# Optimization experiments

Measured on AMD Instinct MI355X. Metric: run time of the kernel, lower is better.

Reference implementation:

```python
import jax, jax.numpy as jnp
import numpy as np

EMBED_DIM = 1024
NUM_HEADS = 16
HEAD_DIM = EMBED_DIM // NUM_HEADS


def setup_inputs() -> dict:
    key = jax.random.key(0)
    ks = jax.random.split(key, 12)
    B, S, D = 2, 2048, EMBED_DIM
    sc = 1.0 / np.sqrt(D)
    inp = {
        "query": jax.random.normal(ks[0], (B, S, D), jnp.float32),
        "key": jax.random.normal(ks[1], (B, S, D), jnp.float32),
        "value": jax.random.normal(ks[2], (B, S, D), jnp.float32),
        # causal mask: True = masked out (matches masked_fill semantics)
        "attn_mask": jnp.triu(jnp.ones((S, S), dtype=bool), k=1),
        "q_w": jax.random.normal(ks[3], (D, D), jnp.float32) * sc,
        "q_b": jnp.zeros((D,), jnp.float32),
        "k_w": jax.random.normal(ks[4], (D, D), jnp.float32) * sc,
        "k_b": jnp.zeros((D,), jnp.float32),
        "v_w": jax.random.normal(ks[5], (D, D), jnp.float32) * sc,
        "v_b": jnp.zeros((D,), jnp.float32),
        "o_w": jax.random.normal(ks[6], (D, D), jnp.float32) * sc,
        "o_b": jnp.zeros((D,), jnp.float32),
    }
    return inp


def reference(query, key, value, attn_mask, q_w, q_b, k_w, k_b, v_w, v_b, o_w, o_b):
    B, S, D = query.shape
    H, hd = NUM_HEADS, HEAD_DIM

    def proj(x, w, b):
        # nn.Linear: x @ w.T + b ; reshape to [B, H, S, hd]
        y = jnp.einsum('bsd,ed->bse', x, w) + b
        return y.reshape(B, S, H, hd).transpose(0, 2, 1, 3)

    Q = proj(query, q_w, q_b)
    K = proj(key, k_w, k_b)
    V = proj(value, v_w, v_b)

    scores = jnp.einsum('bhqd,bhkd->bhqk', Q, K) / jnp.sqrt(jnp.float32(hd))
    scores = jnp.where(attn_mask, jnp.float32(-1e9), scores)
    attn = jax.nn.softmax(scores, axis=-1)  # dropout=0.0 (eval)
    ctx = jnp.einsum('bhqk,bhkd->bhqd', attn, V)
    ctx = ctx.transpose(0, 2, 1, 3).reshape(B, S, D)
    out = jnp.einsum('bsd,ed->bse', ctx, o_w) + o_b
    return out
```

## Files before the change

### kernel.cpp

```cpp
#include <hip/hip_runtime.h>
#include <hip/hip_bf16.h>

typedef __bf16 bf16;
typedef __attribute__((ext_vector_type(8))) __bf16 bf16x8;
typedef __attribute__((ext_vector_type(4))) __bf16 bf16x4;
typedef __attribute__((ext_vector_type(4))) float f32x4;

struct CvtArgs {
  const float* src[7];
  bf16* dst[7];
  int n4[7];
};

__global__ __launch_bounds__(256) void cvt_kernel(CvtArgs a) {
  const int seg = blockIdx.y;
  const float4* s = (const float4*)a.src[seg];
  bf16x4* d = (bf16x4*)a.dst[seg];
  const int n = a.n4[seg];
  const int stride = gridDim.x * 256;
  for (int i = blockIdx.x * 256 + threadIdx.x; i < n; i += stride) {
    const float4 v = s[i];
    bf16x4 h;
    h[0] = (bf16)v.x; h[1] = (bf16)v.y; h[2] = (bf16)v.z; h[3] = (bf16)v.w;
    d[i] = h;
  }
}

__device__ __forceinline__ void gload16(const void* g, void* l) {
  __builtin_amdgcn_global_load_lds(
      (const __attribute__((address_space(1))) void*)g,
      (__attribute__((address_space(3))) void*)l, 16, 0, 0);
}

__device__ __forceinline__ void gemm_core2(const bf16* __restrict__ A,
                                           const bf16* __restrict__ W,
                                           const float* __restrict__ bias,
                                           void* __restrict__ C,
                                           float scale, int mode,
                                           int bx, int by) {
  constexpr int K = 1024, N = 1024, BK = 32, NT = K / BK;
  __shared__ __align__(16) bf16 As[3][128 * BK];
  __shared__ __align__(16) bf16 Bs[3][128 * BK];

  const int tid = threadIdx.x;
  const int lane = tid & 63;
  const int w = tid >> 6;
  const int wm = w >> 1, wn = w & 1;
  const int g = lane >> 4, c16 = lane & 15;
  const int row0 = by * 128;
  const int col0 = bx * 128;

  const int sr = tid >> 2;
  const int ssw = ((tid & 3) ^ (sr & 3)) * 8;
  const int sdst = tid * 8;

  const int aoff = (wm * 64 + c16) * BK + ((g ^ (c16 & 3)) * 8);
  const int boff = (wn * 64 + c16) * BK + ((g ^ (c16 & 3)) * 8);

  f32x4 acc[4][4] = {};

#define STAGE2(buf, kt)                                                          \
  {                                                                              \
    const int k0_ = (kt)*BK;                                                     \
    gload16(&A[(size_t)(row0 + sr) * K + k0_ + ssw], &As[buf][sdst]);            \
    gload16(&A[(size_t)(row0 + 64 + sr) * K + k0_ + ssw], &As[buf][2048 + sdst]);\
    gload16(&W[(size_t)(col0 + sr) * K + k0_ + ssw], &Bs[buf][sdst]);            \
    gload16(&W[(size_t)(col0 + 64 + sr) * K + k0_ + ssw], &Bs[buf][2048 + sdst]);\
  }

  STAGE2(0, 0);
  STAGE2(1, 1);

  int cur = 0;
#pragma unroll 1
  for (int kt = 0; kt < NT; ++kt) {
    if (kt == NT - 1)
      asm volatile("s_waitcnt vmcnt(0)" ::: "memory");
    else
      asm volatile("s_waitcnt vmcnt(4)" ::: "memory");
    __builtin_amdgcn_s_barrier();
    __builtin_amdgcn_sched_barrier(0);

    if (kt + 2 < NT) {
      const int nb = (cur + 2 >= 3) ? cur - 1 : cur + 2;
      STAGE2(nb, kt + 2);
    }

    bf16x8 a[4], b[4];
#pragma unroll
    for (int m = 0; m < 4; ++m) a[m] = *(const bf16x8*)&As[cur][aoff + m * 512];
#pragma unroll
    for (int n = 0; n < 4; ++n) b[n] = *(const bf16x8*)&Bs[cur][boff + n * 512];

    __builtin_amdgcn_s_setprio(1);
#pragma unroll
    for (int m = 0; m < 4; ++m)
#pragma unroll
      for (int n = 0; n < 4; ++n)
        acc[m][n] = __builtin_amdgcn_mfma_f32_16x16x32_bf16(a[m], b[n], acc[m][n], 0, 0, 0);
    __builtin_amdgcn_s_setprio(0);

    cur = (cur + 1 == 3) ? 0 : cur + 1;
  }
#undef STAGE2

#pragma unroll
  for (int m = 0; m < 4; ++m) {
#pragma unroll
    for (int n = 0; n < 4; ++n) {
      const int col = col0 + wn * 64 + n * 16 + c16;
      if (mode == 2) {
        const int row = row0 + wm * 64 + m * 16 + g * 4;
        const int bb = row >> 11, s = row & 2047;
        const int hh = col >> 6, j = col & 63;
        bf16x4 hv;
#pragma unroll
        for (int r = 0; r < 4; ++r)
          hv[r] = (bf16)((acc[m][n][r] + bias[col]) * scale);
        *(bf16x4*)&((bf16*)C)[(((size_t)bb * 16 + hh) * 64 + j) * 2048 + s] = hv;
      } else {
#pragma unroll
        for (int r = 0; r < 4; ++r) {
          const int row = row0 + wm * 64 + m * 16 + g * 4 + r;
          const float v = (acc[m][n][r] + bias[col]) * scale;
          if (mode == 1) {
            const int bb = row >> 11, s = row & 2047;
            const int hh = col >> 6, j = col & 63;
            ((bf16*)C)[(((size_t)bb * 16 + hh) * 2048 + s) * 64 + j] = (bf16)v;
          } else {
            ((float*)C)[(size_t)row * N + col] = v;
          }
        }
      }
    }
  }
}

__device__ __forceinline__ void xcd_swz(int& bx, int& by, int& bz) {
  const int lid = ((int)blockIdx.z * 32 + (int)blockIdx.y) * 8 + (int)blockIdx.x;
  const int cpx = ((int)gridDim.z * 256) >> 3;
  int s = (lid & 7) * cpx + (lid >> 3);
  bx = s & 7;
  by = (s >> 3) & 31;
  bz = s >> 8;
}

__global__ __launch_bounds__(256, 3) void qkv_gemm_kernel(
    const bf16* __restrict__ qa, const bf16* __restrict__ ka, const bf16* __restrict__ va,
    const bf16* __restrict__ qw, const bf16* __restrict__ kw, const bf16* __restrict__ vw,
    const float* __restrict__ qb, const float* __restrict__ kb, const float* __restrict__ vb,
    bf16* __restrict__ Qo, bf16* __restrict__ Ko, bf16* __restrict__ Vo, float qscale) {
  int bx, by, bz;
  xcd_swz(bx, by, bz);
  const bf16* A = (bz == 0) ? qa : (bz == 1) ? ka : va;
  const bf16* W = (bz == 0) ? qw : (bz == 1) ? kw : vw;
  const float* bias = (bz == 0) ? qb : (bz == 1) ? kb : vb;
  bf16* C = (bz == 0) ? Qo : (bz == 1) ? Ko : Vo;
  const float scale = (bz == 0) ? qscale : 1.0f;
  const int mode = (bz == 2) ? 2 : 1;
  gemm_core2(A, W, bias, C, scale, mode, bx, by);
}

__global__ __launch_bounds__(256, 3) void o_gemm_kernel(
    const bf16* __restrict__ A, const bf16* __restrict__ W,
    const float* __restrict__ bias, float* __restrict__ C) {
  int bx, by, bz;
  xcd_swz(bx, by, bz);
  gemm_core2(A, W, bias, C, 1.0f, 0, bx, by);
}

template <bool A_BF16, int OUT_MODE>
__global__ __launch_bounds__(256) void gemm_bt_kernel(
    const void* __restrict__ Aptr, const float* __restrict__ Bt,
    const float* __restrict__ bias, void* __restrict__ Cptr, float scale) {
  constexpr int K = 1024, N = 1024;
  constexpr int BM = 128, BK = 32;
  constexpr int LSTR = BK + 8;
  __shared__ __align__(16) bf16 As[BM][LSTR];
  __shared__ __align__(16) bf16 Bs[BM][LSTR];

  const int tid = threadIdx.x;
  const int lane = tid & 63;
  const int w = tid >> 6;
  const int wr = w >> 1, wc = w & 1;
  const int g = lane >> 4, c16 = lane & 15;
  const int row0 = blockIdx.y * BM;
  const int col0 = blockIdx.x * BM;

  f32x4 acc[4][4] = {};

  for (int kt = 0; kt < K / BK; ++kt) {
    const int k0 = kt * BK;
    if constexpr (!A_BF16) {
      const float* A = (const float*)Aptr;
#pragma unroll
      for (int i = 0; i < 4; ++i) {
        const int r = (tid >> 3) + i * 32;
        const int c = (tid & 7) * 4;
        const float4 v = *(const float4*)(&A[(size_t)(row0 + r) * K + k0 + c]);
        bf16x4 hv;
        hv[0] = (bf16)v.x; hv[1] = (bf16)v.y; hv[2] = (bf16)v.z; hv[3] = (bf16)v.w;
        *(bf16x4*)&As[r][c] = hv;
      }
    } else {
      const bf16* A = (const bf16*)Aptr;
#pragma unroll
      for (int i = 0; i < 2; ++i) {
        const int r = (tid >> 2) + i * 64;
        const int c = (tid & 3) * 8;
        *(bf16x8*)&As[r][c] = *(const bf16x8*)(&A[(size_t)(row0 + r) * K + k0 + c]);
      }
    }
#pragma unroll
    for (int i = 0; i < 4; ++i) {
      const int r = (tid >> 3) + i * 32;
      const int c = (tid & 7) * 4;
      const float4 v = *(const float4*)(&Bt[(size_t)(col0 + r) * K + k0 + c]);
      bf16x4 hv;
      hv[0] = (bf16)v.x; hv[1] = (bf16)v.y; hv[2] = (bf16)v.z; hv[3] = (bf16)v.w;
      *(bf16x4*)&Bs[r][c] = hv;
    }
    __syncthreads();

    bf16x8 a[4], b[4];
#pragma unroll
    for (int m = 0; m < 4; ++m)
      a[m] = *(bf16x8*)&As[wr * 64 + m * 16 + c16][g * 8];
#pragma unroll
    for (int n = 0; n < 4; ++n)
      b[n] = *(bf16x8*)&Bs[wc * 64 + n * 16 + c16][g * 8];
#pragma unroll
    for (int m = 0; m < 4; ++m)
#pragma unroll
      for (int n = 0; n < 4; ++n)
        acc[m][n] = __builtin_amdgcn_mfma_f32_16x16x32_bf16(a[m], b[n], acc[m][n], 0, 0, 0);
    __syncthreads();
  }

#pragma unroll
  for (int m = 0; m < 4; ++m) {
#pragma unroll
    for (int n = 0; n < 4; ++n) {
      const int col = col0 + wc * 64 + n * 16 + c16;
      if constexpr (OUT_MODE == 2) {
        const int row = row0 + wr * 64 + m * 16 + g * 4;
        const int bb = row >> 11, s = row & 2047;
        const int hh = col >> 6, j = col & 63;
        bf16x4 hv;
#pragma unroll
        for (int r = 0; r < 4; ++r)
          hv[r] = (bf16)((acc[m][n][r] + bias[col]) * scale);
        *(bf16x4*)&((bf16*)Cptr)[(((size_t)bb * 16 + hh) * 64 + j) * 2048 + s] = hv;
      } else {
#pragma unroll
        for (int r = 0; r < 4; ++r) {
          const int row = row0 + wr * 64 + m * 16 + g * 4 + r;
          const float v = (acc[m][n][r] + bias[col]) * scale;
          if constexpr (OUT_MODE == 1) {
            const int bb = row >> 11, s = row & 2047;
            const int hh = col >> 6, j = col & 63;
            ((bf16*)Cptr)[(((size_t)bb * 16 + hh) * 2048 + s) * 64 + j] = (bf16)v;
          } else {
            ((float*)Cptr)[(size_t)row * N + col] = v;
          }
        }
      }
    }
  }
}

__global__ __launch_bounds__(256) void attn_kernel(
    const bf16* __restrict__ Q, const bf16* __restrict__ Kb,
    const bf16* __restrict__ Vt, bf16* __restrict__ ctx) {
  constexpr int S = 2048, HD = 64, KVB = 64;
  constexpr int PS = 72;
  __shared__ __align__(16) bf16 Ks[KVB][PS];
  __shared__ __align__(16) bf16 Vs[HD][PS];
  __shared__ __align__(16) bf16 PT[4][16][PS];

  const int tid = threadIdx.x;
  const int lane = tid & 63;
  const int w = tid >> 6;
  const int g = lane >> 4, c16 = lane & 15;
  const int bh = blockIdx.x;
  const int b = bh >> 4, h = bh & 15;

  const int jj = blockIdx.y;
  const int sub = jj & 7, grp = jj >> 3;
  const int qt = (grp == 0) ? sub : (grp == 1) ? 31 - sub : (grp == 2) ? 8 + sub : 23 - sub;

  const bf16* Qh = Q + (size_t)bh * S * HD;
  const bf16* Kh = Kb + (size_t)bh * S * HD;
  const bf16* Vh = Vt + (size_t)bh * HD * S;

  const int srow = tid >> 2;
  const int scol = (tid & 3) * 16;

  const int q0w = qt * 64 + w * 16;
  const int nt = qt + 1;

  bf16x8 qf[2];
#pragma unroll
  for (int ks = 0; ks < 2; ++ks)
    qf[ks] = *(const bf16x8*)&Qh[(size_t)(q0w + c16) * HD + ks * 32 + g * 8];

  f32x4 oacc[4] = {};
  float m = -1e30f, l = 0.f;

  bf16x8 kr0 = *(const bf16x8*)&Kh[(size_t)srow * HD + scol];
  bf16x8 kr1 = *(const bf16x8*)&Kh[(size_t)srow * HD + scol + 8];
  bf16x8 vr0 = *(const bf16x8*)&Vh[(size_t)srow * S + scol];
  bf16x8 vr1 = *(const bf16x8*)&Vh[(size_t)srow * S + scol + 8];

#pragma unroll 1
  for (int kt = 0; kt < nt; ++kt) {
    __syncthreads();
    *(bf16x8*)&Ks[srow][scol] = kr0;
    *(bf16x8*)&Ks[srow][scol + 8] = kr1;
    *(bf16x8*)&Vs[srow][scol] = vr0;
    *(bf16x8*)&Vs[srow][scol + 8] = vr1;
    __syncthreads();

    const int kv0 = kt * KVB;
    const bool pf = (kt + 1 < nt);
    if (pf) {
      const int nkv = kv0 + KVB;
      kr0 = *(const bf16x8*)&Kh[(size_t)(nkv + srow) * HD + scol];
      kr1 = *(const bf16x8*)&Kh[(size_t)(nkv + srow) * HD + scol + 8];
      vr0 = *(const bf16x8*)&Vh[(size_t)srow * S + nkv + scol];
      vr1 = *(const bf16x8*)&Vh[(size_t)srow * S + nkv + scol + 8];
    }

    f32x4 sc[4] = {};
    __builtin_amdgcn_s_setprio(1);
#pragma unroll
    for (int ks = 0; ks < 2; ++ks) {
#pragma unroll
      for (int ni = 0; ni < 4; ++ni) {
        const bf16x8 kf = *(const bf16x8*)&Ks[ni * 16 + c16][ks * 32 + g * 8];
        sc[ni] = __builtin_amdgcn_mfma_f32_16x16x32_bf16(kf, qf[ks], sc[ni], 0, 0, 0);
      }
    }
    __builtin_amdgcn_s_setprio(0);

    if (kt == qt) {
      const int qq = q0w + c16;
#pragma unroll
      for (int ni = 0; ni < 4; ++ni)
#pragma unroll
        for (int r = 0; r < 4; ++r) {
          const int kv = kv0 + ni * 16 + g * 4 + r;
          if (kv > qq) sc[ni][r] = -1e30f;
        }
    }

    float t = -1e30f;
#pragma unroll
    for (int ni = 0; ni < 4; ++ni)
#pragma unroll
      for (int r = 0; r < 4; ++r) t = fmaxf(t, sc[ni][r]);
    t = fmaxf(t, __shfl_xor(t, 16));
    t = fmaxf(t, __shfl_xor(t, 32));
    if (!__all(t <= m + 8.0f)) {
      const float mnew = fmaxf(m, t);
      const float corr = exp2f(m - mnew);
      m = mnew;
      l *= corr;
      float cb[4];
#pragma unroll
      for (int r = 0; r < 4; ++r)
        cb[r] = __shfl(corr, (lane & 48) + g * 4 + r);
#pragma unroll
      for (int nd = 0; nd < 4; ++nd)
#pragma unroll
        for (int r = 0; r < 4; ++r) oacc[nd][r] *= cb[r];
    }
    float rs = 0.f;
#pragma unroll
    for (int ni = 0; ni < 4; ++ni)
#pragma unroll
      for (int r = 0; r < 4; ++r) {
        sc[ni][r] = exp2f(sc[ni][r] - m);
        rs += sc[ni][r];
      }
    rs += __shfl_xor(rs, 16);
    rs += __shfl_xor(rs, 32);
    l += rs;

#pragma unroll
    for (int ni = 0; ni < 4; ++ni) {
      bf16x4 hv;
#pragma unroll
      for (int r = 0; r < 4; ++r) hv[r] = (bf16)sc[ni][r];
      *(bf16x4*)&PT[w][c16][ni * 16 + g * 4] = hv;
    }

    __builtin_amdgcn_s_setprio(1);
#pragma unroll
    for (int ks = 0; ks < 2; ++ks) {
      const bf16x8 pa = *(const bf16x8*)&PT[w][c16][ks * 32 + g * 8];
#pragma unroll
      for (int nd = 0; nd < 4; ++nd) {
        const bf16x8 bv = *(const bf16x8*)&Vs[nd * 16 + c16][ks * 32 + g * 8];
        oacc[nd] = __builtin_amdgcn_mfma_f32_16x16x32_bf16(pa, bv, oacc[nd], 0, 0, 0);
      }
    }
    __builtin_amdgcn_s_setprio(0);
  }

  float lb[4];
#pragma unroll
  for (int r = 0; r < 4; ++r)
    lb[r] = __shfl(l, (lane & 48) + g * 4 + r);
#pragma unroll
  for (int nd = 0; nd < 4; ++nd)
#pragma unroll
    for (int r = 0; r < 4; ++r) {
      const int q = q0w + g * 4 + r;
      const int col = h * 64 + nd * 16 + c16;
      ctx[((size_t)b * S + q) * 1024 + col] = (bf16)(oacc[nd][r] / lb[r]);
    }
}

extern "C" void kernel_launch(void* const* d_in, const int* in_sizes, int n_in,
                              void* d_out, int out_size, void* d_ws, size_t ws_size,
                              hipStream_t stream) {
  (void)in_sizes; (void)n_in; (void)out_size;
  const float* query = (const float*)d_in[0];
  const float* key   = (const float*)d_in[1];
  const float* value = (const float*)d_in[2];
  const float* q_w = (const float*)d_in[4];
  const float* q_b = (const float*)d_in[5];
  const float* k_w = (const float*)d_in[6];
  const float* k_b = (const float*)d_in[7];
  const float* v_w = (const float*)d_in[8];
  const float* v_b = (const float*)d_in[9];
  const float* o_w = (const float*)d_in[10];
  const float* o_b = (const float*)d_in[11];

  const size_t NELEM = (size_t)4096 * 1024;
  const size_t WELEM = (size_t)1024 * 1024;
  bf16* Qbuf = (bf16*)d_ws;
  bf16* Kbuf = Qbuf + NELEM;
  bf16* Vbuf = Kbuf + NELEM;
  bf16* ctxb = Vbuf + NELEM;

  const dim3 blk(256);
  const float QSCALE = 0.125f * 1.44269504088896f;

  const size_t need = 64ull * 1024 * 1024;
  if (ws_size >= need) {
    bf16* qbf  = ctxb + NELEM;
    bf16* kbf  = qbf + NELEM;
    bf16* vbf  = kbf + NELEM;
    bf16* qwbf = vbf + NELEM;
    bf16* kwbf = qwbf + WELEM;
    bf16* vwbf = kwbf + WELEM;
    bf16* owbf = vwbf + WELEM;

    CvtArgs ca;
    ca.src[0] = query; ca.dst[0] = qbf;  ca.n4[0] = (int)(NELEM / 4);
    ca.src[1] = key;   ca.dst[1] = kbf;  ca.n4[1] = (int)(NELEM / 4);
    ca.src[2] = value; ca.dst[2] = vbf;  ca.n4[2] = (int)(NELEM / 4);
    ca.src[3] = q_w;   ca.dst[3] = qwbf; ca.n4[3] = (int)(WELEM / 4);
    ca.src[4] = k_w;   ca.dst[4] = kwbf; ca.n4[4] = (int)(WELEM / 4);
    ca.src[5] = v_w;   ca.dst[5] = vwbf; ca.n4[5] = (int)(WELEM / 4);
    ca.src[6] = o_w;   ca.dst[6] = owbf; ca.n4[6] = (int)(WELEM / 4);
    cvt_kernel<<<dim3(256, 7), blk, 0, stream>>>(ca);

    qkv_gemm_kernel<<<dim3(8, 32, 3), blk, 0, stream>>>(
        qbf, kbf, vbf, qwbf, kwbf, vwbf, q_b, k_b, v_b, Qbuf, Kbuf, Vbuf, QSCALE);

    attn_kernel<<<dim3(32, 32), blk, 0, stream>>>(Qbuf, Kbuf, Vbuf, ctxb);

    o_gemm_kernel<<<dim3(8, 32), blk, 0, stream>>>(ctxb, owbf, o_b, (float*)d_out);
  } else {
    const dim3 ggrid(8, 32);
    gemm_bt_kernel<false, 1><<<ggrid, blk, 0, stream>>>(query, q_w, q_b, Qbuf, QSCALE);
    gemm_bt_kernel<false, 1><<<ggrid, blk, 0, stream>>>(key, k_w, k_b, Kbuf, 1.0f);
    gemm_bt_kernel<false, 2><<<ggrid, blk, 0, stream>>>(value, v_w, v_b, Vbuf, 1.0f);
    attn_kernel<<<dim3(32, 32), blk, 0, stream>>>(Qbuf, Kbuf, Vbuf, ctxb);
    gemm_bt_kernel<true, 0><<<ggrid, blk, 0, stream>>>(ctxb, o_w, o_b, d_out, 1.0f);
  }
}
```

Baseline: 124.6 us.

## Load K/V fragments directly from global memory, dropping shared-memory staging and barriers

```diff
diff --git a/kernel.cpp b/kernel.cpp
--- a/kernel.cpp
+++ b/kernel.cpp
@@ -269,13 +269,11 @@
   }
 }
 
-__global__ __launch_bounds__(256) void attn_kernel(
+__global__ __launch_bounds__(256, 4) void attn_kernel(
     const bf16* __restrict__ Q, const bf16* __restrict__ Kb,
     const bf16* __restrict__ Vt, bf16* __restrict__ ctx) {
   constexpr int S = 2048, HD = 64, KVB = 64;
   constexpr int PS = 72;
-  __shared__ __align__(16) bf16 Ks[KVB][PS];
-  __shared__ __align__(16) bf16 Vs[HD][PS];
   __shared__ __align__(16) bf16 PT[4][16][PS];
 
   const int tid = threadIdx.x;
@@ -293,9 +291,6 @@
   const bf16* Kh = Kb + (size_t)bh * S * HD;
   const bf16* Vh = Vt + (size_t)bh * HD * S;
 
-  const int srow = tid >> 2;
-  const int scol = (tid & 3) * 16;
-
   const int q0w = qt * 64 + w * 16;
   const int nt = qt + 1;
 
@@ -307,41 +302,32 @@
   f32x4 oacc[4] = {};
   float m = -1e30f, l = 0.f;
 
-  bf16x8 kr0 = *(const bf16x8*)&Kh[(size_t)srow * HD + scol];
-  bf16x8 kr1 = *(const bf16x8*)&Kh[(size_t)srow * HD + scol + 8];
-  bf16x8 vr0 = *(const bf16x8*)&Vh[(size_t)srow * S + scol];
-  bf16x8 vr1 = *(const bf16x8*)&Vh[(size_t)srow * S + scol + 8];
-
 #pragma unroll 1
   for (int kt = 0; kt < nt; ++kt) {
-    __syncthreads();
-    *(bf16x8*)&Ks[srow][scol] = kr0;
-    *(bf16x8*)&Ks[srow][scol + 8] = kr1;
-    *(bf16x8*)&Vs[srow][scol] = vr0;
-    *(bf16x8*)&Vs[srow][scol + 8] = vr1;
-    __syncthreads();
-
     const int kv0 = kt * KVB;
-    const bool pf = (kt + 1 < nt);
-    if (pf) {
-      const int nkv = kv0 + KVB;
-      kr0 = *(const bf16x8*)&Kh[(size_t)(nkv + srow) * HD + scol];
-      kr1 = *(const bf16x8*)&Kh[(size_t)(nkv + srow) * HD + scol + 8];
-      vr0 = *(const bf16x8*)&Vh[(size_t)srow * S + nkv + scol];
-      vr1 = *(const bf16x8*)&Vh[(size_t)srow * S + nkv + scol + 8];
-    }
+
+    bf16x8 kf[4][2];
+#pragma unroll
+    for (int ni = 0; ni < 4; ++ni)
+#pragma unroll
+      for (int ks = 0; ks < 2; ++ks)
+        kf[ni][ks] = *(const bf16x8*)&Kh[(size_t)(kv0 + ni * 16 + c16) * HD + ks * 32 + g * 8];
 
     f32x4 sc[4] = {};
     __builtin_amdgcn_s_setprio(1);
 #pragma unroll
-    for (int ks = 0; ks < 2; ++ks) {
-#pragma unroll
-      for (int ni = 0; ni < 4; ++ni) {
-        const bf16x8 kf = *(const bf16x8*)&Ks[ni * 16 + c16][ks * 32 + g * 8];
-        sc[ni] = __builtin_amdgcn_mfma_f32_16x16x32_bf16(kf, qf[ks], sc[ni], 0, 0, 0);
-      }
-    }
+    for (int ks = 0; ks < 2; ++ks)
+#pragma unroll
+      for (int ni = 0; ni < 4; ++ni)
+        sc[ni] = __builtin_amdgcn_mfma_f32_16x16x32_bf16(kf[ni][ks], qf[ks], sc[ni], 0, 0, 0);
     __builtin_amdgcn_s_setprio(0);
+
+    bf16x8 bv[2][4];
+#pragma unroll
+    for (int ks = 0; ks < 2; ++ks)
+#pragma unroll
+      for (int nd = 0; nd < 4; ++nd)
+        bv[ks][nd] = *(const bf16x8*)&Vh[(size_t)(nd * 16 + c16) * S + kv0 + ks * 32 + g * 8];
 
     if (kt == qt) {
       const int qq = q0w + c16;
@@ -400,10 +386,8 @@
     for (int ks = 0; ks < 2; ++ks) {
       const bf16x8 pa = *(const bf16x8*)&PT[w][c16][ks * 32 + g * 8];
 #pragma unroll
-      for (int nd = 0; nd < 4; ++nd) {
-        const bf16x8 bv = *(const bf16x8*)&Vs[nd * 16 + c16][ks * 32 + g * 8];
-        oacc[nd] = __builtin_amdgcn_mfma_f32_16x16x32_bf16(pa, bv, oacc[nd], 0, 0, 0);
-      }
+      for (int nd = 0; nd < 4; ++nd)
+        oacc[nd] = __builtin_amdgcn_mfma_f32_16x16x32_bf16(pa, bv[ks][nd], oacc[nd], 0, 0, 0);
     }
     __builtin_amdgcn_s_setprio(0);
   }
```

Result: slower. 196.3 us (+57.5%).
